# Kernel optimization log

Measured on AMD Instinct MI355X. Metric: run time of the kernel, lower is better.

The kernel has to match this reference:

```python
import jax, jax.numpy as jnp
import numpy as np

B, S, H, G, DH = 2, 2048, 16, 4, 64
D = H * DH        # 1024
DKV = G * DH      # 256
SCALE = 1.0 / np.sqrt(DH).astype(np.float32)


def apply_rope(x, rope):
    # x: [..., S, DH]; rope: [2, S, DH] (rope[0]=cos, rope[1]=sin)
    xr = x.reshape(*x.shape[:-1], DH // 2, 2)
    x_rot = jnp.stack([-xr[..., 1], xr[..., 0]], axis=-1).reshape(x.shape)
    return x * rope[0] + x_rot * rope[1]


def setup_inputs() -> dict:
    key = jax.random.key(0)
    ks = jax.random.split(key, 5)
    X = jax.random.normal(ks[0], (B, S, D), dtype=jnp.float32)
    Wq = jax.random.normal(ks[1], (D, D), dtype=jnp.float32) / np.sqrt(D).astype(np.float32)
    Wk = jax.random.normal(ks[2], (DKV, D), dtype=jnp.float32) / np.sqrt(D).astype(np.float32)
    Wv = jax.random.normal(ks[3], (DKV, D), dtype=jnp.float32) / np.sqrt(D).astype(np.float32)
    Wo = jax.random.normal(ks[4], (D, D), dtype=jnp.float32) / np.sqrt(D).astype(np.float32)
    # standard RoPE angles, interleaved (pairs (0,1),(2,3),...)
    pos = jnp.arange(S, dtype=jnp.float32)
    inv_freq = 1.0 / (10000.0 ** (jnp.arange(0, DH, 2, dtype=jnp.float32) / DH))
    ang = pos[:, None] * inv_freq[None, :]          # [S, DH/2]
    ang = jnp.repeat(ang, 2, axis=-1)               # [S, DH]
    rope = jnp.stack([jnp.cos(ang), jnp.sin(ang)])  # [2, S, DH]
    causal = jnp.tril(jnp.ones((S, S), dtype=bool))
    return {"X": X, "Wq": Wq, "Wk": Wk, "Wv": Wv, "Wo": Wo, "rope": rope, "causal": causal}


def reference(X, Wq, Wk, Wv, Wo, rope, causal):
    # QKV projections (torch Linear: y = x @ W.T)
    Q = (X @ Wq.T).reshape(B, S, H, DH).transpose(0, 2, 1, 3)   # [B,H,S,DH]
    K = (X @ Wk.T).reshape(B, S, G, DH).transpose(0, 2, 1, 3)   # [B,G,S,DH]
    V = (X @ Wv.T).reshape(B, S, G, DH).transpose(0, 2, 1, 3)   # [B,G,S,DH]
    Q = apply_rope(Q, rope)
    K = apply_rope(K, rope)
    # GQA: repeat KV heads (repeat_interleave semantics)
    K = jnp.repeat(K, H // G, axis=1)                            # [B,H,S,DH]
    V = jnp.repeat(V, H // G, axis=1)
    scores = SCALE * jnp.einsum('bhqd,bhkd->bhqk', Q, K)         # [B,H,S,S]
    scores = jnp.where(causal, scores, -jnp.inf)
    A = jax.nn.softmax(scores, axis=-1)
    Y = jnp.einsum('bhqk,bhkd->bhqd', A, V)                      # [B,H,S,DH]
    Y = Y.transpose(0, 2, 1, 3).reshape(B, S, D)
    return Y @ Wo.T
```

## Files before the change

### kernel.cpp

```cpp
#include <hip/hip_runtime.h>
#include <hip/hip_bf16.h>

#define B_   2
#define S_   2048
#define H_   16
#define G_   4
#define DH_  64
#define D_   1024
#define DKV_ 256
#define SCALE_ 0.125f
#define LDQK_ 1280

using short8  = __attribute__((ext_vector_type(8))) short;
using floatx4 = __attribute__((ext_vector_type(4))) float;
typedef unsigned short ushort_t;

__device__ __forceinline__ ushort_t f2bf(float f) {
    union { float f; unsigned u; } v; v.f = f;
    unsigned r = v.u + 0x7fffu + ((v.u >> 16) & 1u);
    return (ushort_t)(r >> 16);
}
__device__ __forceinline__ float bf2f(ushort_t u) {
    union { unsigned u; float f; } v; v.u = ((unsigned)u) << 16;
    return v.f;
}
__device__ __forceinline__ unsigned cvt_pk_bf16(float lo, float hi) {
    unsigned r;
    asm("v_cvt_pk_bf16_f32 %0, %1, %2" : "=v"(r) : "v"(lo), "v"(hi));
    return r;
}

__device__ __forceinline__ void gload16(const ushort_t* g, ushort_t* l) {
    __builtin_amdgcn_global_load_lds(
        (const __attribute__((address_space(1))) void*)g,
        (__attribute__((address_space(3))) void*)l, 16, 0, 0);
}

__global__ void pack_all(const float* __restrict__ X,  const float* __restrict__ Wq,
                         const float* __restrict__ Wk, const float* __restrict__ Wv,
                         const float* __restrict__ Wo, ushort_t* __restrict__ dst) {
    const int X4  = B_ * S_ * D_ / 4;
    const int QW4 = D_ * D_ / 4;
    const int KW4 = DKV_ * D_ / 4;
    int i = blockIdx.x * blockDim.x + threadIdx.x;
    const float* src; int off;
    if (i < X4)                        { src = X;  off = i; }
    else if (i < X4 + QW4)             { src = Wq; off = i - X4; }
    else if (i < X4 + QW4 + KW4)       { src = Wk; off = i - X4 - QW4; }
    else if (i < X4 + QW4 + 2 * KW4)   { src = Wv; off = i - X4 - QW4 - KW4; }
    else                               { src = Wo; off = i - X4 - QW4 - 2 * KW4; }
    float4 v = reinterpret_cast<const float4*>(src)[off];
    ushort4 o;
    o.x = f2bf(v.x); o.y = f2bf(v.y); o.z = f2bf(v.z); o.w = f2bf(v.w);
    reinterpret_cast<ushort4*>(dst)[i] = o;
}

template<int MODE>
__global__ __launch_bounds__(256)
void gemm_all(const ushort_t* __restrict__ Xb,  const ushort_t* __restrict__ Wqkb,
              const ushort_t* __restrict__ Wvb, const ushort_t* __restrict__ Wob,
              ushort_t* __restrict__ QKb, ushort_t* __restrict__ Vtb,
              const ushort_t* __restrict__ Yb, float* __restrict__ Cout,
              const float* __restrict__ rope, float qscale)
{
    __shared__ __align__(16) ushort_t Asm[2][128 * 64];
    __shared__ __align__(16) ushort_t Bsm[2][64 * 64];

    const ushort_t *Aorig, *Borig;
    ushort_t* Cb = nullptr; float* Cf = nullptr;
    int m0, n0, ldc, epi;
    if (MODE == 1) {
        const int f = blockIdx.x + 32 * blockIdx.y;
        const int xcd = f & 7, j = f >> 3;
        m0 = (xcd + 8 * (j & 3)) * 128;
        n0 = (j >> 2) * 64;
        Aorig = Yb; Borig = Wob; Cf = Cout; ldc = D_; epi = 1;
    } else {
        const int f = blockIdx.x;
        if (f < 640) {
            const int xcd = f & 7, j = f >> 3;
            m0 = (xcd + 8 * (j & 3)) * 128;
            n0 = (j >> 2) * 64;
            Aorig = Xb; Borig = Wqkb; Cb = QKb; ldc = LDQK_; epi = 2;
        } else {
            const int idx = f - 640, b = idx >> 6, rem = idx & 63;
            m0 = (rem >> 5) * 128; n0 = (rem & 31) * 64;
            Aorig = Wvb; Borig = Xb + (long)b * S_ * D_;
            Cb = Vtb + (long)b * DKV_ * S_; ldc = S_; epi = 0;
        }
    }

    const int tid = threadIdx.x, l = tid & 63, w = tid >> 6;
    const int wr = (w >> 1) * 64, wc = (w & 1) * 32;
    const int lr = l & 15, lkb = l >> 4;

    const int srow = w * 8 + (l >> 3);
    const int scol = ((l & 7) ^ ((l >> 3) & 7)) * 8;
    const ushort_t* Ast = Aorig + (long)(m0 + srow) * D_ + scol;
    const ushort_t* Bst = Borig + (long)(n0 + srow) * D_ + scol;

#define GSTAGE(buf, kt)                                                    \
    {                                                                      \
        _Pragma("unroll")                                                  \
        for (int rr = 0; rr < 4; ++rr)                                     \
            gload16(Ast + (long)rr * 32 * D_ + (kt), &Asm[buf][w * 512 + rr * 2048]); \
        _Pragma("unroll")                                                  \
        for (int c = 0; c < 2; ++c)                                        \
            gload16(Bst + (long)c * 32 * D_ + (kt), &Bsm[buf][w * 512 + c * 2048]);   \
    }

    floatx4 acc[4][2] = {};
    const int xr = (lr & 7) << 4;
    GSTAGE(0, 0);
    for (int i = 0; i < 16; ++i) {
        const int cur = i & 1;
        if (i < 15) {
            GSTAGE(cur ^ 1, (i + 1) * 64);
            asm volatile("s_waitcnt vmcnt(6)" ::: "memory");
        } else {
            asm volatile("s_waitcnt vmcnt(0)" ::: "memory");
        }
        __builtin_amdgcn_s_barrier();

#pragma unroll
        for (int ks = 0; ks < 2; ++ks) {
            short8 a[4], bb[2];
#pragma unroll
            for (int ii = 0; ii < 4; ++ii) {
                const int row = wr + ii * 16 + lr;
                a[ii] = *(const short8*)&Asm[cur][(row * 128 + ((ks * 64 + lkb * 16) ^ xr)) >> 1];
            }
#pragma unroll
            for (int j = 0; j < 2; ++j) {
                const int row = wc + j * 16 + lr;
                bb[j] = *(const short8*)&Bsm[cur][(row * 128 + ((ks * 64 + lkb * 16) ^ xr)) >> 1];
            }
            __builtin_amdgcn_s_setprio(1);
#pragma unroll
            for (int ii = 0; ii < 4; ++ii)
#pragma unroll
                for (int j = 0; j < 2; ++j)
                    acc[ii][j] = __builtin_amdgcn_mfma_f32_16x16x32_bf16(a[ii], bb[j], acc[ii][j], 0, 0, 0);
            __builtin_amdgcn_s_setprio(0);
        }
        __builtin_amdgcn_s_barrier();
    }
#undef GSTAGE

    const int rrow = lkb * 4;
#pragma unroll
    for (int i = 0; i < 4; ++i) {
#pragma unroll
        for (int j = 0; j < 2; ++j) {
#pragma unroll
            for (int r = 0; r < 4; ++r) {
                const int row = m0 + wr + i * 16 + rrow + r;
                const int col = n0 + wc + j * 16 + lr;
                if (epi == 1) {
                    Cf[(long)row * ldc + col] = acc[i][j][r];
                } else if (epi == 0) {
                    Cb[(long)row * ldc + col] = f2bf(acc[i][j][r]);
                } else {
                    const float v  = acc[i][j][r];
                    const float pv = __shfl_xor(v, 1);
                    const int   s  = row & (S_ - 1);
                    const int   d  = col & (DH_ - 1);
                    const float cc = rope[s * DH_ + d];
                    const float sn = rope[S_ * DH_ + s * DH_ + d];
                    float res = (lr & 1) ? (v * cc + pv * sn) : (v * cc - pv * sn);
                    res *= (col < D_) ? qscale : 1.0f;
                    Cb[(long)row * ldc + col] = f2bf(res);
                }
            }
        }
    }
}

__global__ __launch_bounds__(512)
void attn_kernel(const ushort_t* __restrict__ QK, const ushort_t* __restrict__ Vt,
                 ushort_t* __restrict__ Y0, ushort_t* __restrict__ Y1,
                 float* __restrict__ L0, float* __restrict__ L1)
{
    __shared__ __align__(16) ushort_t Kt [4][64 * 64];
    __shared__ __align__(16) ushort_t Vts[4][64 * 64];

    const int tid = threadIdx.x;
    const int l   = tid & 63;
    const int w   = tid >> 6;
    const int lr  = l & 15, lkb = l >> 4, lk = lkb * 8;

    const int f   = blockIdx.x + 16 * (blockIdx.y + 16 * blockIdx.z);
    const int xcd = f & 7, j = f >> 3;
    const int b   = xcd >> 2;
    const int g   = xcd & 3;
    const int h   = g * 4 + (j & 3);
    const int bx  = j >> 2;

    const int sr  = l >> 3;
    const int sce = ((l & 7) ^ sr) * 8;
    const ushort_t* Ksrc = QK + (long)b * S_ * LDQK_ + D_ + g * DH_ + sce;
    const ushort_t* Vsrc = Vt + (long)(b * G_ + g) * DH_ * S_ + sce;

    const int rl = w * 8 + sr;
    const int kr = (rl & 0x23) | ((rl & 0x0C) << 1) | ((rl & 0x10) >> 2);

    short8 vones;
#pragma unroll
    for (int jj = 0; jj < 8; ++jj) vones[jj] = (short)0x3F80;

#define STG(bi, tt)                                                       \
    {                                                                     \
        gload16(Ksrc + (long)((tt) * 64 + kr) * LDQK_, &Kt[bi][w * 512]); \
        gload16(Vsrc + (long)rl * S_ + (tt) * 64,      &Vts[bi][w * 512]);\
    }

    for (int seg = 0; seg < 2; ++seg) {
        const int qt = seg == 0 ? (S_ / 128 - 1 - bx) : bx;
        const int t0 = seg == 0 ? qt + 1 : 0;
        const int n  = qt + 1;
        const int tmax = t0 + n - 1;
        const int qrow0 = qt * 128 + w * 16;

        const ushort_t* Qp = QK + ((long)b * S_ + qrow0 + lr) * LDQK_ + h * DH_ + lk;
        const short8 bq0 = *(const short8*)(Qp);
        const short8 bq1 = *(const short8*)(Qp + 32);

        floatx4 o[4] = {};
        floatx4 osum = {};

        auto compute_tile = [&](int cur, int t) {
            floatx4 sacc[4] = {};
            __builtin_amdgcn_s_setprio(1);
#pragma unroll
            for (int cf = 0; cf < 4; ++cf) {
                const int row = cf * 16 + lr;
                const int xr  = (row & 7) << 4;
                const short8 ak0 = *(const short8*)&Kt[cur][(row * 128 + ((lkb * 16) ^ xr)) >> 1];
                const short8 ak1 = *(const short8*)&Kt[cur][(row * 128 + ((64 + lkb * 16) ^ xr)) >> 1];
                sacc[cf] = __builtin_amdgcn_mfma_f32_16x16x32_bf16(ak0, bq0, sacc[cf], 0, 0, 0);
                sacc[cf] = __builtin_amdgcn_mfma_f32_16x16x32_bf16(ak1, bq1, sacc[cf], 0, 0, 0);
            }
            __builtin_amdgcn_s_setprio(0);

            if (t >= 2 * qt) {
                const int qg = qrow0 + lr;
#pragma unroll
                for (int cf = 0; cf < 4; ++cf) {
                    const int kvb0 = t * 64 + 32 * (cf >> 1) + 8 * lkb + 4 * (cf & 1);
#pragma unroll
                    for (int r = 0; r < 4; ++r)
                        if (kvb0 + r > qg) sacc[cf][r] = -3e38f;
                }
            }

#pragma unroll
            for (int cf = 0; cf < 4; ++cf)
#pragma unroll
                for (int r = 0; r < 4; ++r)
                    sacc[cf][r] = exp2f(sacc[cf][r]);

#pragma unroll
            for (int ks = 0; ks < 2; ++ks) {
                union { unsigned u[4]; short8 s; } pa;
#pragma unroll
                for (int jj = 0; jj < 4; ++jj) {
                    const int cf = 2 * ks + (jj >> 1);
                    const int e  = (jj & 1) * 2;
                    pa.u[jj] = cvt_pk_bf16(sacc[cf][e], sacc[cf][e + 1]);
                }
                __builtin_amdgcn_s_setprio(1);
#pragma unroll
                for (int df = 0; df < 4; ++df) {
                    const int vrow = df * 16 + lr;
                    const int xr   = (vrow & 7) << 4;
                    const short8 bv = *(const short8*)&Vts[cur][(vrow * 128 + ((ks * 64 + lkb * 16) ^ xr)) >> 1];
                    o[df] = __builtin_amdgcn_mfma_f32_16x16x32_bf16(pa.s, bv, o[df], 0, 0, 0);
                }
                osum = __builtin_amdgcn_mfma_f32_16x16x32_bf16(pa.s, vones, osum, 0, 0, 0);
                __builtin_amdgcn_s_setprio(0);
            }
        };

        STG(0, t0);
        STG(1, (t0 + 1 <= tmax) ? t0 + 1 : tmax);

        for (int i = 0; i < n; i += 2) {
            const int tn2 = (t0 + i + 2 <= tmax) ? t0 + i + 2 : tmax;
            const int tn3 = (t0 + i + 3 <= tmax) ? t0 + i + 3 : tmax;
            STG((i + 2) & 3, tn2);
            STG((i + 3) & 3, tn3);
            asm volatile("s_waitcnt vmcnt(4)" ::: "memory");
            __builtin_amdgcn_s_barrier();
            compute_tile(i & 3, t0 + i);
            if (i + 1 < n) compute_tile((i + 1) & 3, t0 + i + 1);
            __builtin_amdgcn_s_barrier();
        }
        asm volatile("s_waitcnt vmcnt(0)" ::: "memory");

        ushort_t* Yp = seg == 0 ? Y1 : Y0;
        float*    Lp = seg == 0 ? L1 : L0;
#pragma unroll
        for (int r = 0; r < 4; ++r) {
            const int row = qrow0 + lkb * 4 + r;
#pragma unroll
            for (int df = 0; df < 4; ++df)
                Yp[((long)b * S_ + row) * D_ + h * DH_ + df * 16 + lr] = f2bf(o[df][r]);
            if (lr == 0)
                Lp[((long)b * S_ + row) * H_ + h] = osum[r];
        }
        __builtin_amdgcn_s_barrier();
    }
#undef STG
}

__global__ void combine_kernel(ushort_t* __restrict__ Y0, const ushort_t* __restrict__ Y1,
                               const float* __restrict__ L0, const float* __restrict__ L1) {
    const int i  = blockIdx.x * blockDim.x + threadIdx.x;
    const int row = i >> 7;
    const int h   = (i & 127) >> 3;
    const float inv = 1.f / (L0[row * H_ + h] + L1[row * H_ + h]);
    const short8 y0 = ((const short8*)Y0)[i];
    const short8 y1 = ((const short8*)Y1)[i];
    union { unsigned u[4]; short8 s; } o;
#pragma unroll
    for (int j = 0; j < 4; ++j) {
        const float a = (bf2f((ushort_t)y0[2 * j])     + bf2f((ushort_t)y1[2 * j]))     * inv;
        const float c = (bf2f((ushort_t)y0[2 * j + 1]) + bf2f((ushort_t)y1[2 * j + 1])) * inv;
        o.u[j] = cvt_pk_bf16(a, c);
    }
    ((short8*)Y0)[i] = o.s;
}

extern "C" void kernel_launch(void* const* d_in, const int* in_sizes, int n_in,
                              void* d_out, int out_size, void* d_ws, size_t ws_size,
                              hipStream_t stream) {
    const float* X    = (const float*)d_in[0];
    const float* Wq   = (const float*)d_in[1];
    const float* Wk   = (const float*)d_in[2];
    const float* Wv   = (const float*)d_in[3];
    const float* Wo   = (const float*)d_in[4];
    const float* rope = (const float*)d_in[5];
    float* out = (float*)d_out;

    char* ws = (char*)d_ws;
    size_t o = 0;
    ushort_t* Xb   = (ushort_t*)(ws + o); o += (size_t)B_ * S_ * D_ * 2;
    ushort_t* Wqkb = (ushort_t*)(ws + o); o += (size_t)LDQK_ * D_ * 2;
    ushort_t* Wvb  = (ushort_t*)(ws + o); o += (size_t)DKV_ * D_ * 2;
    ushort_t* Wob  = (ushort_t*)(ws + o); o += (size_t)D_ * D_ * 2;
    ushort_t* QKb  = (ushort_t*)(ws + o); o += (size_t)B_ * S_ * LDQK_ * 2;
    ushort_t* Vtb  = (ushort_t*)(ws + o); o += (size_t)B_ * G_ * DH_ * S_ * 2;
    ushort_t* Y1b  = (ushort_t*)(ws + o); o += (size_t)B_ * S_ * D_ * 2;
    float*    L0   = (float*)(ws + o);    o += (size_t)B_ * S_ * H_ * 4;
    float*    L1   = (float*)(ws + o);    o += (size_t)B_ * S_ * H_ * 4;
    ushort_t* Y0   = Xb;

    {
        int n4 = (B_ * S_ * D_ + 2 * D_ * D_ + 2 * DKV_ * D_) / 4;
        pack_all<<<(n4 + 255) / 256, 256, 0, stream>>>(X, Wq, Wk, Wv, Wo, Xb);
    }

    const float SC2 = SCALE_ * 1.44269504f;
    gemm_all<0><<<dim3(768, 1, 1), 256, 0, stream>>>(
        Xb, Wqkb, Wvb, Wob, QKb, Vtb, nullptr, nullptr, rope, SC2);

    attn_kernel<<<dim3(S_ / 128, H_, B_), 512, 0, stream>>>(QKb, Vtb, Y0, Y1b, L0, L1);

    {
        int nthr = B_ * S_ * D_ / 8;
        combine_kernel<<<nthr / 256, 256, 0, stream>>>(Y0, Y1b, L0, L1);
    }

    gemm_all<1><<<dim3(32, 16, 1), 256, 0, stream>>>(
        Xb, Wqkb, Wvb, Wob, QKb, Vtb, Y0, out, nullptr, 0.f);
}
```

Before: 93.41 us.

## Halve attention block to 4 waves, each wave processing 32 query rows

The attention kernel now runs 256 threads per block instead of 512. Each wave handles two 16-row query sub-tiles and reuses every K and V fragment read from LDS for both. Each thread issues twice as many staging loads, and the wait count is adjusted to match. This cuts LDS reads per MFMA and barrier participants, at the cost of more registers per wave and fewer waves to hide latency.

```diff
diff --git a/kernel.cpp b/kernel.cpp
--- a/kernel.cpp
+++ b/kernel.cpp
@@ -176,7 +176,7 @@
     }
 }
 
-__global__ __launch_bounds__(512)
+__global__ __launch_bounds__(256)
 void attn_kernel(const ushort_t* __restrict__ QK, const ushort_t* __restrict__ Vt,
                  ushort_t* __restrict__ Y0, ushort_t* __restrict__ Y1,
                  float* __restrict__ L0, float* __restrict__ L1)
@@ -201,17 +201,21 @@
     const ushort_t* Ksrc = QK + (long)b * S_ * LDQK_ + D_ + g * DH_ + sce;
     const ushort_t* Vsrc = Vt + (long)(b * G_ + g) * DH_ * S_ + sce;
 
-    const int rl = w * 8 + sr;
-    const int kr = (rl & 0x23) | ((rl & 0x0C) << 1) | ((rl & 0x10) >> 2);
+    const int rl0 = w * 16 + sr;
+    const int rl1 = w * 16 + 8 + sr;
+    const int kr0 = (rl0 & 0x23) | ((rl0 & 0x0C) << 1) | ((rl0 & 0x10) >> 2);
+    const int kr1 = (rl1 & 0x23) | ((rl1 & 0x0C) << 1) | ((rl1 & 0x10) >> 2);
 
     short8 vones;
 #pragma unroll
     for (int jj = 0; jj < 8; ++jj) vones[jj] = (short)0x3F80;
 
-#define STG(bi, tt)                                                       \
-    {                                                                     \
-        gload16(Ksrc + (long)((tt) * 64 + kr) * LDQK_, &Kt[bi][w * 512]); \
-        gload16(Vsrc + (long)rl * S_ + (tt) * 64,      &Vts[bi][w * 512]);\
+#define STG(bi, tt)                                                         \
+    {                                                                       \
+        gload16(Ksrc + (long)((tt) * 64 + kr0) * LDQK_, &Kt[bi][w * 1024]); \
+        gload16(Ksrc + (long)((tt) * 64 + kr1) * LDQK_, &Kt[bi][w * 1024 + 512]); \
+        gload16(Vsrc + (long)rl0 * S_ + (tt) * 64,      &Vts[bi][w * 1024]);      \
+        gload16(Vsrc + (long)rl1 * S_ + (tt) * 64,      &Vts[bi][w * 1024 + 512]);\
     }
 
     for (int seg = 0; seg < 2; ++seg) {
@@ -219,17 +223,21 @@
         const int t0 = seg == 0 ? qt + 1 : 0;
         const int n  = qt + 1;
         const int tmax = t0 + n - 1;
-        const int qrow0 = qt * 128 + w * 16;
-
-        const ushort_t* Qp = QK + ((long)b * S_ + qrow0 + lr) * LDQK_ + h * DH_ + lk;
-        const short8 bq0 = *(const short8*)(Qp);
-        const short8 bq1 = *(const short8*)(Qp + 32);
-
-        floatx4 o[4] = {};
-        floatx4 osum = {};
+        const int qrow0 = qt * 128 + w * 32;
+
+        short8 bq[2][2];
+#pragma unroll
+        for (int qs = 0; qs < 2; ++qs) {
+            const ushort_t* Qp = QK + ((long)b * S_ + qrow0 + qs * 16 + lr) * LDQK_ + h * DH_ + lk;
+            bq[qs][0] = *(const short8*)(Qp);
+            bq[qs][1] = *(const short8*)(Qp + 32);
+        }
+
+        floatx4 o[2][4] = {};
+        floatx4 osum[2] = {};
 
         auto compute_tile = [&](int cur, int t) {
-            floatx4 sacc[4] = {};
+            floatx4 sacc[2][4] = {};
             __builtin_amdgcn_s_setprio(1);
 #pragma unroll
             for (int cf = 0; cf < 4; ++cf) {
@@ -237,46 +245,58 @@
                 const int xr  = (row & 7) << 4;
                 const short8 ak0 = *(const short8*)&Kt[cur][(row * 128 + ((lkb * 16) ^ xr)) >> 1];
                 const short8 ak1 = *(const short8*)&Kt[cur][(row * 128 + ((64 + lkb * 16) ^ xr)) >> 1];
-                sacc[cf] = __builtin_amdgcn_mfma_f32_16x16x32_bf16(ak0, bq0, sacc[cf], 0, 0, 0);
-                sacc[cf] = __builtin_amdgcn_mfma_f32_16x16x32_bf16(ak1, bq1, sacc[cf], 0, 0, 0);
+#pragma unroll
+                for (int qs = 0; qs < 2; ++qs) {
+                    sacc[qs][cf] = __builtin_amdgcn_mfma_f32_16x16x32_bf16(ak0, bq[qs][0], sacc[qs][cf], 0, 0, 0);
+                    sacc[qs][cf] = __builtin_amdgcn_mfma_f32_16x16x32_bf16(ak1, bq[qs][1], sacc[qs][cf], 0, 0, 0);
+                }
             }
             __builtin_amdgcn_s_setprio(0);
 
             if (t >= 2 * qt) {
-                const int qg = qrow0 + lr;
-#pragma unroll
-                for (int cf = 0; cf < 4; ++cf) {
-                    const int kvb0 = t * 64 + 32 * (cf >> 1) + 8 * lkb + 4 * (cf & 1);
+#pragma unroll
+                for (int qs = 0; qs < 2; ++qs) {
+                    const int qg = qrow0 + qs * 16 + lr;
+#pragma unroll
+                    for (int cf = 0; cf < 4; ++cf) {
+                        const int kvb0 = t * 64 + 32 * (cf >> 1) + 8 * lkb + 4 * (cf & 1);
+#pragma unroll
+                        for (int r = 0; r < 4; ++r)
+                            if (kvb0 + r > qg) sacc[qs][cf][r] = -3e38f;
+                    }
+                }
+            }
+
+#pragma unroll
+            for (int qs = 0; qs < 2; ++qs)
+#pragma unroll
+                for (int cf = 0; cf < 4; ++cf)
 #pragma unroll
                     for (int r = 0; r < 4; ++r)
-                        if (kvb0 + r > qg) sacc[cf][r] = -3e38f;
-                }
-            }
-
-#pragma unroll
-            for (int cf = 0; cf < 4; ++cf)
-#pragma unroll
-                for (int r = 0; r < 4; ++r)
-                    sacc[cf][r] = exp2f(sacc[cf][r]);
+                        sacc[qs][cf][r] = exp2f(sacc[qs][cf][r]);
 
 #pragma unroll
             for (int ks = 0; ks < 2; ++ks) {
-                union { unsigned u[4]; short8 s; } pa;
-#pragma unroll
-                for (int jj = 0; jj < 4; ++jj) {
-                    const int cf = 2 * ks + (jj >> 1);
-                    const int e  = (jj & 1) * 2;
-                    pa.u[jj] = cvt_pk_bf16(sacc[cf][e], sacc[cf][e + 1]);
-                }
+                union { unsigned u[4]; short8 s; } pa[2];
+#pragma unroll
+                for (int qs = 0; qs < 2; ++qs)
+#pragma unroll
+                    for (int jj = 0; jj < 4; ++jj) {
+                        const int cf = 2 * ks + (jj >> 1);
+                        const int e  = (jj & 1) * 2;
+                        pa[qs].u[jj] = cvt_pk_bf16(sacc[qs][cf][e], sacc[qs][cf][e + 1]);
+                    }
                 __builtin_amdgcn_s_setprio(1);
 #pragma unroll
                 for (int df = 0; df < 4; ++df) {
                     const int vrow = df * 16 + lr;
                     const int xr   = (vrow & 7) << 4;
                     const short8 bv = *(const short8*)&Vts[cur][(vrow * 128 + ((ks * 64 + lkb * 16) ^ xr)) >> 1];
-                    o[df] = __builtin_amdgcn_mfma_f32_16x16x32_bf16(pa.s, bv, o[df], 0, 0, 0);
+                    o[0][df] = __builtin_amdgcn_mfma_f32_16x16x32_bf16(pa[0].s, bv, o[0][df], 0, 0, 0);
+                    o[1][df] = __builtin_amdgcn_mfma_f32_16x16x32_bf16(pa[1].s, bv, o[1][df], 0, 0, 0);
                 }
-                osum = __builtin_amdgcn_mfma_f32_16x16x32_bf16(pa.s, vones, osum, 0, 0, 0);
+                osum[0] = __builtin_amdgcn_mfma_f32_16x16x32_bf16(pa[0].s, vones, osum[0], 0, 0, 0);
+                osum[1] = __builtin_amdgcn_mfma_f32_16x16x32_bf16(pa[1].s, vones, osum[1], 0, 0, 0);
                 __builtin_amdgcn_s_setprio(0);
             }
         };
@@ -289,7 +309,7 @@
             const int tn3 = (t0 + i + 3 <= tmax) ? t0 + i + 3 : tmax;
             STG((i + 2) & 3, tn2);
             STG((i + 3) & 3, tn3);
-            asm volatile("s_waitcnt vmcnt(4)" ::: "memory");
+            asm volatile("s_waitcnt vmcnt(8)" ::: "memory");
             __builtin_amdgcn_s_barrier();
             compute_tile(i & 3, t0 + i);
             if (i + 1 < n) compute_tile((i + 1) & 3, t0 + i + 1);
@@ -300,14 +320,16 @@
         ushort_t* Yp = seg == 0 ? Y1 : Y0;
         float*    Lp = seg == 0 ? L1 : L0;
 #pragma unroll
-        for (int r = 0; r < 4; ++r) {
-            const int row = qrow0 + lkb * 4 + r;
-#pragma unroll
-            for (int df = 0; df < 4; ++df)
-                Yp[((long)b * S_ + row) * D_ + h * DH_ + df * 16 + lr] = f2bf(o[df][r]);
-            if (lr == 0)
-                Lp[((long)b * S_ + row) * H_ + h] = osum[r];
-        }
+        for (int qs = 0; qs < 2; ++qs)
+#pragma unroll
+            for (int r = 0; r < 4; ++r) {
+                const int row = qrow0 + qs * 16 + lkb * 4 + r;
+#pragma unroll
+                for (int df = 0; df < 4; ++df)
+                    Yp[((long)b * S_ + row) * D_ + h * DH_ + df * 16 + lr] = f2bf(o[qs][df][r]);
+                if (lr == 0)
+                    Lp[((long)b * S_ + row) * H_ + h] = osum[qs][r];
+            }
         __builtin_amdgcn_s_barrier();
     }
 #undef STG
@@ -364,7 +386,7 @@
     gemm_all<0><<<dim3(768, 1, 1), 256, 0, stream>>>(
         Xb, Wqkb, Wvb, Wob, QKb, Vtb, nullptr, nullptr, rope, SC2);
 
-    attn_kernel<<<dim3(S_ / 128, H_, B_), 512, 0, stream>>>(QKb, Vtb, Y0, Y1b, L0, L1);
+    attn_kernel<<<dim3(S_ / 128, H_, B_), 256, 0, stream>>>(QKb, Vtb, Y0, Y1b, L0, L1);
 
     {
         int nthr = B_ * S_ * D_ / 8;
```

After: 96.84 us. 1.04x slower.
